# Optimization experiments

Measured on AMD Instinct MI355X. Metric: run time of the kernel, lower is better.

## Reference

```python
import jax, jax.numpy as jnp
import numpy as np
import math

HIDDEN_DIM = 1024
NUM_MODALITIES = 8
NUM_HEADS = 8
HEAD_DIM = HIDDEN_DIM // NUM_HEADS
LN_EPS = 1e-5


def setup_inputs() -> dict:
    key = jax.random.key(0)
    ks = jax.random.split(key, 12)
    B, K, D = 8192, NUM_MODALITIES, HIDDEN_DIM
    s = 1.0 / math.sqrt(D)
    inp = {
        'modality_encodings': jax.random.normal(ks[0], (B, K, D), dtype=jnp.float32),
        'selection_mask': jnp.ones((B, K), dtype=jnp.float32),
        # nn.Linear weights are [out, in]
        'wq': jax.random.uniform(ks[1], (D, D), jnp.float32, -s, s),
        'bq': jax.random.uniform(ks[2], (D,), jnp.float32, -s, s),
        'wk': jax.random.uniform(ks[3], (D, D), jnp.float32, -s, s),
        'bk': jax.random.uniform(ks[4], (D,), jnp.float32, -s, s),
        'wv': jax.random.uniform(ks[5], (D, D), jnp.float32, -s, s),
        'bv': jax.random.uniform(ks[6], (D,), jnp.float32, -s, s),
        'wo': jax.random.uniform(ks[7], (D, D), jnp.float32, -s, s),
        'bo': jax.random.uniform(ks[8], (D,), jnp.float32, -s, s),
        'rel_prior': jnp.eye(K, dtype=jnp.float32) + 0.1 * jax.random.normal(ks[9], (K, K), dtype=jnp.float32),
        'ln_gamma': jnp.ones((D,), dtype=jnp.float32),
        'ln_beta': jnp.zeros((D,), dtype=jnp.float32),
    }
    return inp


def reference(modality_encodings, selection_mask, wq, bq, wk, bk, wv, bv, wo, bo,
              rel_prior, ln_gamma, ln_beta):
    x = modality_encodings  # [B, K, D]
    B, K, D = x.shape
    H, Hd = NUM_HEADS, HEAD_DIM

    def lin(t, w, b):
        return t @ w.T + b

    def heads(t):  # [B,K,D] -> [B,H,K,Hd]
        return t.reshape(B, K, H, Hd).transpose(0, 2, 1, 3)

    q = heads(lin(x, wq, bq))
    k = heads(lin(x, wk, bk))
    v = heads(lin(x, wv, bv))

    scores = jnp.einsum('bhqd,bhkd->bhqk', q, k) / math.sqrt(Hd)
    scores = scores + rel_prior[None, None, :, :]  # learned additive bias

    # selection mask: mask_2d[b,q,k] = mask[b,q]*mask[b,k]; fill -inf where 0
    mask_2d = (selection_mask[:, :, None] * selection_mask[:, None, :]) > 0  # [B,K,K]
    scores = jnp.where(mask_2d[:, None, :, :], scores, -jnp.inf)

    attn = jax.nn.softmax(scores, axis=-1)
    # dropout(p=0.1) in eval mode -> identity
    out = jnp.einsum('bhqk,bhkd->bhqd', attn, v)  # [B,H,K,Hd]
    out = out.transpose(0, 2, 1, 3).reshape(B, K, D)
    out = lin(out, wo, bo)

    res = x + out
    mu = jnp.mean(res, axis=-1, keepdims=True)
    var = jnp.mean(jnp.square(res - mu), axis=-1, keepdims=True)
    return (res - mu) * jax.lax.rsqrt(var + LN_EPS) * ln_gamma + ln_beta
```

## Files before the change

### kernel.cpp

```cpp
#include <hip/hip_runtime.h>

typedef __attribute__((ext_vector_type(4))) float f32x4;
typedef __attribute__((ext_vector_type(8))) short short8;

#define LN_EPS 1e-5f

__device__ __forceinline__ float bf2f(short x) {
  union { unsigned u; float f; } c;
  c.u = ((unsigned)(unsigned short)x) << 16;
  return c.f;
}
__device__ __forceinline__ short f2b(float f) {
  union { float f; unsigned u; } c; c.f = f;
  unsigned r = (c.u + 0x7fffu + ((c.u >> 16) & 1u)) >> 16;
  return (short)r;
}

__global__ __launch_bounds__(256) void cvt_kernel(const float* __restrict__ src,
                                                  short* __restrict__ dst, int n8) {
  int idx = blockIdx.x * 256 + threadIdx.x;
  int stride = gridDim.x * 256;
  for (int c = idx; c < n8; c += stride) {
    const f32x4* s = (const f32x4*)(src + (size_t)c * 8);
    f32x4 v0 = s[0], v1 = s[1];
    short8 o;
    o[0] = f2b(v0.x); o[1] = f2b(v0.y); o[2] = f2b(v0.z); o[3] = f2b(v0.w);
    o[4] = f2b(v1.x); o[5] = f2b(v1.y); o[6] = f2b(v1.z); o[7] = f2b(v1.w);
    *(short8*)(dst + (size_t)c * 8) = o;
  }
}

__global__ __launch_bounds__(256) void pack_bias(const float* __restrict__ bq,
                                                 const float* __restrict__ bk,
                                                 const float* __restrict__ bv,
                                                 float* __restrict__ dst) {
  int t = blockIdx.x * 256 + threadIdx.x;
  if (t < 1024) { dst[t] = bq[t]; dst[1024 + t] = bk[t]; dst[2048 + t] = bv[t]; }
}

__device__ __forceinline__ void gload16(const short* g, const short* l) {
  __builtin_amdgcn_global_load_lds((const __attribute__((address_space(1))) unsigned int*)g,
                                   (__attribute__((address_space(3))) unsigned int*)l,
                                   16, 0, 0);
}

template <int MODE>
__global__ __launch_bounds__(512, 2) void gemm256(
    const short* __restrict__ A, const short* __restrict__ W,
    const float* __restrict__ bias, const float* __restrict__ resid,
    void* __restrict__ Cptr, int N) {
  __shared__ __align__(16) short lds[65536];

  const int tid = threadIdx.x;
  const int w = tid >> 6, l = tid & 63;
  const int wr = w >> 2, wc = w & 3;
  const int r0 = l & 15, hk = l >> 4;

  const int q8 = gridDim.x >> 3;
  const int wg = (blockIdx.x & 7) * q8 + (blockIdx.x >> 3);
  const int nbx = N >> 8;
  const int mb = wg / nbx, nb = wg - mb * nbx;
  const int m0 = mb << 8, n0 = nb << 8;

  const int srow = tid >> 3;
  const int colsh = (((tid & 7) ^ (srow & 7)) << 3);
  const short* gA00 = A + (size_t)(m0 + srow) * 1024 + colsh;
  const short* gA01 = A + (size_t)(m0 + srow + 64) * 1024 + colsh;
  const short* gA10 = A + (size_t)(m0 + 128 + srow) * 1024 + colsh;
  const short* gA11 = A + (size_t)(m0 + 128 + srow + 64) * 1024 + colsh;
  const short* gB00 = W + (size_t)(n0 + srow) * 1024 + colsh;
  const short* gB01 = W + (size_t)(n0 + srow + 64) * 1024 + colsh;
  const short* gB10 = W + (size_t)(n0 + 128 + srow) * 1024 + colsh;
  const short* gB11 = W + (size_t)(n0 + 128 + srow + 64) * 1024 + colsh;
  const int wofs = w * 512;

  const int ps0 = hk ^ (r0 & 7);
  const int aO0 = r0 * 64 + ps0 * 8;
  const int aO1 = r0 * 64 + (ps0 ^ 4) * 8;
  const int rB = (wc & 1) * 64;
  const int bO0 = (rB + r0) * 64 + ps0 * 8;
  const int bO1 = (rB + r0) * 64 + (ps0 ^ 4) * 8;
  const short* Abase = &lds[wr * 8192];
  const short* Bbase = &lds[32768 + (wc >> 1) * 8192];

  f32x4 acc[8][4];
#pragma unroll
  for (int i = 0; i < 8; ++i)
#pragma unroll
    for (int j = 0; j < 4; ++j) acc[i][j] = (f32x4)(0.f);

  gload16(gA00, &lds[wofs]);
  gload16(gA01, &lds[wofs + 4096]);
  gload16(gA10, &lds[8192 + wofs]);
  gload16(gA11, &lds[8192 + wofs + 4096]);
  gload16(gB00, &lds[32768 + wofs]);
  gload16(gB01, &lds[32768 + wofs + 4096]);
  gload16(gB10, &lds[32768 + 8192 + wofs]);
  gload16(gB11, &lds[32768 + 8192 + wofs + 4096]);

#pragma unroll 2
  for (int t = 0; t < 16; ++t) {
    const int p = t & 1;
    const short* Ab = Abase + p * 16384;
    const short* Bb = Bbase + p * 16384;
    short8 av[4][2], bw[4][2];

    __builtin_amdgcn_sched_barrier(0);
    asm volatile("s_waitcnt vmcnt(0)" ::: "memory");
    __builtin_amdgcn_s_barrier();
    __builtin_amdgcn_sched_barrier(0);
#pragma unroll
    for (int i4 = 0; i4 < 4; ++i4) {
      av[i4][0] = *(const short8*)&Ab[aO0 + i4 * 1024];
      av[i4][1] = *(const short8*)&Ab[aO1 + i4 * 1024];
    }
#pragma unroll
    for (int j = 0; j < 2; ++j) {
      bw[j][0] = *(const short8*)&Bb[bO0 + j * 1024];
      bw[j][1] = *(const short8*)&Bb[bO1 + j * 1024];
    }
    if (t < 15) {
      const int kofs = (t + 1) * 64;
      const int qb = (p ^ 1) * 16384;
      gload16(gA00 + kofs, &lds[qb + wofs]);
      gload16(gA01 + kofs, &lds[qb + wofs + 4096]);
      gload16(gA10 + kofs, &lds[qb + 8192 + wofs]);
      gload16(gA11 + kofs, &lds[qb + 8192 + wofs + 4096]);
      gload16(gB00 + kofs, &lds[32768 + qb + wofs]);
      gload16(gB01 + kofs, &lds[32768 + qb + wofs + 4096]);
      gload16(gB10 + kofs, &lds[32768 + qb + 8192 + wofs]);
      gload16(gB11 + kofs, &lds[32768 + qb + 8192 + wofs + 4096]);
    }
    __builtin_amdgcn_s_setprio(1);
#pragma unroll
    for (int ks = 0; ks < 2; ++ks)
#pragma unroll
      for (int i4 = 0; i4 < 4; ++i4)
#pragma unroll
        for (int j = 0; j < 2; ++j)
          acc[i4][j] = __builtin_amdgcn_mfma_f32_16x16x32_bf16(av[i4][ks], bw[j][ks], acc[i4][j], 0, 0, 0);
    __builtin_amdgcn_s_setprio(0);

    __builtin_amdgcn_s_barrier();
    __builtin_amdgcn_sched_barrier(0);
#pragma unroll
    for (int j = 2; j < 4; ++j) {
      bw[j][0] = *(const short8*)&Bb[bO0 + j * 1024];
      bw[j][1] = *(const short8*)&Bb[bO1 + j * 1024];
    }
    __builtin_amdgcn_s_setprio(1);
#pragma unroll
    for (int ks = 0; ks < 2; ++ks)
#pragma unroll
      for (int i4 = 0; i4 < 4; ++i4)
#pragma unroll
        for (int j = 2; j < 4; ++j)
          acc[i4][j] = __builtin_amdgcn_mfma_f32_16x16x32_bf16(av[i4][ks], bw[j][ks], acc[i4][j], 0, 0, 0);
    __builtin_amdgcn_s_setprio(0);

    __builtin_amdgcn_s_barrier();
    __builtin_amdgcn_sched_barrier(0);
#pragma unroll
    for (int i4 = 0; i4 < 4; ++i4) {
      av[i4][0] = *(const short8*)&Ab[aO0 + (4 + i4) * 1024];
      av[i4][1] = *(const short8*)&Ab[aO1 + (4 + i4) * 1024];
    }
    __builtin_amdgcn_s_setprio(1);
#pragma unroll
    for (int ks = 0; ks < 2; ++ks)
#pragma unroll
      for (int i4 = 0; i4 < 4; ++i4)
#pragma unroll
        for (int j = 2; j < 4; ++j)
          acc[4 + i4][j] = __builtin_amdgcn_mfma_f32_16x16x32_bf16(av[i4][ks], bw[j][ks], acc[4 + i4][j], 0, 0, 0);
    __builtin_amdgcn_s_setprio(0);

    __builtin_amdgcn_s_barrier();
    __builtin_amdgcn_sched_barrier(0);
    __builtin_amdgcn_s_setprio(1);
#pragma unroll
    for (int ks = 0; ks < 2; ++ks)
#pragma unroll
      for (int i4 = 0; i4 < 4; ++i4)
#pragma unroll
        for (int j = 0; j < 2; ++j)
          acc[4 + i4][j] = __builtin_amdgcn_mfma_f32_16x16x32_bf16(av[i4][ks], bw[j][ks], acc[4 + i4][j], 0, 0, 0);
    __builtin_amdgcn_s_setprio(0);
  }

  const int crow = m0 + wr * 128 + hk * 4;
  const int ccol = n0 + wc * 64 + r0;
  if (MODE == 0) {
    short* C = (short*)Cptr;
#pragma unroll
    for (int j = 0; j < 4; ++j) {
      float bj = bias[ccol + j * 16];
#pragma unroll
      for (int i = 0; i < 8; ++i) {
        size_t base = (size_t)(crow + i * 16) * N + (ccol + j * 16);
#pragma unroll
        for (int rr = 0; rr < 4; ++rr)
          C[base + (size_t)rr * N] = f2b(acc[i][j][rr] + bj);
      }
    }
  } else {
    float* C = (float*)Cptr;
#pragma unroll
    for (int j = 0; j < 4; ++j) {
      float bj = bias[ccol + j * 16];
#pragma unroll
      for (int i = 0; i < 8; ++i) {
        size_t base = (size_t)(crow + i * 16) * N + (ccol + j * 16);
#pragma unroll
        for (int rr = 0; rr < 4; ++rr)
          C[base + (size_t)rr * N] =
              acc[i][j][rr] + bj + resid[base + (size_t)rr * N];
      }
    }
  }
}

__global__ __launch_bounds__(256) void attn_kernel(
    const short* __restrict__ qkv, const float* __restrict__ prior,
    const float* __restrict__ mask, short* __restrict__ out) {
  __shared__ short sq[8 * 3080];
  const int tid = threadIdx.x;
  const int b = blockIdx.x;
  for (int c = tid; c < 3072; c += 256) {
    int row = c / 384;
    int cc = c - row * 384;
    *(short8*)&sq[row * 3080 + cc * 8] =
        *(const short8*)&qkv[((size_t)b * 8 + row) * 3072 + cc * 8];
  }
  __syncthreads();
  const int l = tid & 63, w = tid >> 6;
  const int i = l >> 3, j = l & 7;
  const float pv = prior[l];
  const float mm = mask[b * 8 + i] * mask[b * 8 + j];
#pragma unroll
  for (int hh = 0; hh < 2; ++hh) {
    const int h = w + hh * 4;
    const short* Qr = &sq[i * 3080 + h * 128];
    const short* Kr = &sq[j * 3080 + 1024 + h * 128];
    float s = 0.f;
#pragma unroll
    for (int c = 0; c < 16; ++c) {
      short8 qa = *(const short8*)&Qr[c * 8];
      short8 ka = *(const short8*)&Kr[c * 8];
#pragma unroll
      for (int e = 0; e < 8; ++e) s += bf2f(qa[e]) * bf2f(ka[e]);
    }
    s = s * 0.08838834764831843f + pv;
    if (!(mm > 0.f)) s = -__builtin_inff();
    float mx = s;
#pragma unroll
    for (int off = 1; off < 8; off <<= 1) mx = fmaxf(mx, __shfl_xor(mx, off));
    float e = __expf(s - mx);
    float sum = e;
#pragma unroll
    for (int off = 1; off < 8; off <<= 1) sum += __shfl_xor(sum, off);
    float p = e / sum;
    float o[16];
#pragma unroll
    for (int t = 0; t < 16; ++t) o[t] = 0.f;
#pragma unroll
    for (int jj = 0; jj < 8; ++jj) {
      float pj = __shfl(p, i * 8 + jj);
      const short* Vr = &sq[jj * 3080 + 2048 + h * 128 + j * 16];
      short8 v0 = *(const short8*)&Vr[0];
      short8 v1 = *(const short8*)&Vr[8];
#pragma unroll
      for (int e2 = 0; e2 < 8; ++e2) {
        o[e2] += pj * bf2f(v0[e2]);
        o[8 + e2] += pj * bf2f(v1[e2]);
      }
    }
    short8 o0, o1;
#pragma unroll
    for (int e2 = 0; e2 < 8; ++e2) { o0[e2] = f2b(o[e2]); o1[e2] = f2b(o[8 + e2]); }
    short* dst = out + ((size_t)(b * 8 + i)) * 1024 + h * 128 + j * 16;
    *(short8*)dst = o0;
    *(short8*)(dst + 8) = o1;
  }
}

__global__ __launch_bounds__(256) void ln_kernel(float* __restrict__ io,
                                                 const float* __restrict__ gamma,
                                                 const float* __restrict__ beta) {
  const int l = threadIdx.x & 63, w = threadIdx.x >> 6;
  float* p = io + ((size_t)blockIdx.x * 4 + w) * 1024;
  f32x4 v[4];
  float s = 0.f;
#pragma unroll
  for (int c = 0; c < 4; ++c) {
    v[c] = *(const f32x4*)(p + (c * 64 + l) * 4);
    s += v[c][0] + v[c][1] + v[c][2] + v[c][3];
  }
#pragma unroll
  for (int off = 32; off > 0; off >>= 1) s += __shfl_xor(s, off);
  const float mu = s * (1.f / 1024.f);
  float s2 = 0.f;
#pragma unroll
  for (int c = 0; c < 4; ++c)
#pragma unroll
    for (int e = 0; e < 4; ++e) { float d = v[c][e] - mu; s2 += d * d; }
#pragma unroll
  for (int off = 32; off > 0; off >>= 1) s2 += __shfl_xor(s2, off);
  const float rstd = rsqrtf(s2 * (1.f / 1024.f) + LN_EPS);
#pragma unroll
  for (int c = 0; c < 4; ++c) {
    f32x4 g = *(const f32x4*)(gamma + (c * 64 + l) * 4);
    f32x4 bt = *(const f32x4*)(beta + (c * 64 + l) * 4);
    f32x4 ov;
#pragma unroll
    for (int e = 0; e < 4; ++e) ov[e] = (v[c][e] - mu) * rstd * g[e] + bt[e];
    *(f32x4*)(p + (c * 64 + l) * 4) = ov;
  }
}

extern "C" void kernel_launch(void* const* d_in, const int* in_sizes, int n_in,
                              void* d_out, int out_size, void* d_ws, size_t ws_size,
                              hipStream_t stream) {
  const float* x     = (const float*)d_in[0];
  const float* mask  = (const float*)d_in[1];
  const float* wq    = (const float*)d_in[2];
  const float* bq    = (const float*)d_in[3];
  const float* wk    = (const float*)d_in[4];
  const float* bk    = (const float*)d_in[5];
  const float* wv    = (const float*)d_in[6];
  const float* bv    = (const float*)d_in[7];
  const float* wo    = (const float*)d_in[8];
  const float* bo    = (const float*)d_in[9];
  const float* prior = (const float*)d_in[10];
  const float* gamma = (const float*)d_in[11];
  const float* beta  = (const float*)d_in[12];

  char* ws = (char*)d_ws;
  short* qkv  = (short*)(ws);
  short* xb   = (short*)(ws + 402653184L);
  short* wall = (short*)(ws + 536870912L);
  short* wob  = (short*)(ws + 543162368L);
  float* ball = (float*)(ws + 545259520L);

  cvt_kernel<<<2048, 256, 0, stream>>>(x, xb, 8388608);
  cvt_kernel<<<512, 256, 0, stream>>>(wq, wall,           131072);
  cvt_kernel<<<512, 256, 0, stream>>>(wk, wall + 1048576, 131072);
  cvt_kernel<<<512, 256, 0, stream>>>(wv, wall + 2097152, 131072);
  cvt_kernel<<<512, 256, 0, stream>>>(wo, wob,            131072);
  pack_bias<<<4, 256, 0, stream>>>(bq, bk, bv, ball);

  gemm256<0><<<3072, 512, 0, stream>>>(xb, wall, ball, nullptr, qkv, 3072);
  attn_kernel<<<8192, 256, 0, stream>>>(qkv, prior, mask, xb);
  gemm256<1><<<1024, 512, 0, stream>>>(xb, wob, bo, x, d_out, 1024);
  ln_kernel<<<16384, 256, 0, stream>>>((float*)d_out, gamma, beta);
}
```

Measured before the change: 1.005 ms.

## Prefetch GEMM tiles two steps ahead within the double buffer

The GEMM main loop now stages tiles t and t+1 up front. It issues the global-to-LDS loads for tile t+2 into the current buffer once each operand's last LDS reads in the iteration have passed a barrier: B after the third phase, A after the fourth. The per-iteration wait drops from vmcnt(0) to vmcnt(8), so only the older tile's loads must complete and one tile's loads stay in flight across the barrier. The aim is to hide more global-memory latency behind MFMA work. The cost is more outstanding memory operations and a vmcnt-based ordering that is easy to get wrong.

```diff
diff --git a/kernel.cpp b/kernel.cpp
--- a/kernel.cpp
+++ b/kernel.cpp
@@ -74,6 +74,17 @@
   const short* gB11 = W + (size_t)(n0 + 128 + srow + 64) * 1024 + colsh;
   const int wofs = w * 512;
 
+#define STAGE_A(T, BUF) do { const int kofs_ = (T) * 64, qb_ = (BUF) * 16384;       \
+    gload16(gA00 + kofs_, &lds[qb_ + wofs]);                                        \
+    gload16(gA01 + kofs_, &lds[qb_ + wofs + 4096]);                                 \
+    gload16(gA10 + kofs_, &lds[qb_ + 8192 + wofs]);                                 \
+    gload16(gA11 + kofs_, &lds[qb_ + 8192 + wofs + 4096]); } while (0)
+#define STAGE_B(T, BUF) do { const int kofs_ = (T) * 64, qb_ = (BUF) * 16384;       \
+    gload16(gB00 + kofs_, &lds[32768 + qb_ + wofs]);                                \
+    gload16(gB01 + kofs_, &lds[32768 + qb_ + wofs + 4096]);                         \
+    gload16(gB10 + kofs_, &lds[32768 + qb_ + 8192 + wofs]);                         \
+    gload16(gB11 + kofs_, &lds[32768 + qb_ + 8192 + wofs + 4096]); } while (0)
+
   const int ps0 = hk ^ (r0 & 7);
   const int aO0 = r0 * 64 + ps0 * 8;
   const int aO1 = r0 * 64 + (ps0 ^ 4) * 8;
@@ -89,14 +100,8 @@
 #pragma unroll
     for (int j = 0; j < 4; ++j) acc[i][j] = (f32x4)(0.f);
 
-  gload16(gA00, &lds[wofs]);
-  gload16(gA01, &lds[wofs + 4096]);
-  gload16(gA10, &lds[8192 + wofs]);
-  gload16(gA11, &lds[8192 + wofs + 4096]);
-  gload16(gB00, &lds[32768 + wofs]);
-  gload16(gB01, &lds[32768 + wofs + 4096]);
-  gload16(gB10, &lds[32768 + 8192 + wofs]);
-  gload16(gB11, &lds[32768 + 8192 + wofs + 4096]);
+  STAGE_A(0, 0); STAGE_B(0, 0);
+  STAGE_A(1, 1); STAGE_B(1, 1);
 
 #pragma unroll 2
   for (int t = 0; t < 16; ++t) {
@@ -106,7 +111,8 @@
     short8 av[4][2], bw[4][2];
 
     __builtin_amdgcn_sched_barrier(0);
-    asm volatile("s_waitcnt vmcnt(0)" ::: "memory");
+    if (t == 15) { asm volatile("s_waitcnt vmcnt(0)" ::: "memory"); }
+    else         { asm volatile("s_waitcnt vmcnt(8)" ::: "memory"); }
     __builtin_amdgcn_s_barrier();
     __builtin_amdgcn_sched_barrier(0);
 #pragma unroll
@@ -119,18 +125,6 @@
       bw[j][0] = *(const short8*)&Bb[bO0 + j * 1024];
       bw[j][1] = *(const short8*)&Bb[bO1 + j * 1024];
     }
-    if (t < 15) {
-      const int kofs = (t + 1) * 64;
-      const int qb = (p ^ 1) * 16384;
-      gload16(gA00 + kofs, &lds[qb + wofs]);
-      gload16(gA01 + kofs, &lds[qb + wofs + 4096]);
-      gload16(gA10 + kofs, &lds[qb + 8192 + wofs]);
-      gload16(gA11 + kofs, &lds[qb + 8192 + wofs + 4096]);
-      gload16(gB00 + kofs, &lds[32768 + qb + wofs]);
-      gload16(gB01 + kofs, &lds[32768 + qb + wofs + 4096]);
-      gload16(gB10 + kofs, &lds[32768 + qb + 8192 + wofs]);
-      gload16(gB11 + kofs, &lds[32768 + qb + 8192 + wofs + 4096]);
-    }
     __builtin_amdgcn_s_setprio(1);
 #pragma unroll
     for (int ks = 0; ks < 2; ++ks)
@@ -165,6 +159,7 @@
       av[i4][0] = *(const short8*)&Ab[aO0 + (4 + i4) * 1024];
       av[i4][1] = *(const short8*)&Ab[aO1 + (4 + i4) * 1024];
     }
+    if (t < 14) STAGE_B(t + 2, p);
     __builtin_amdgcn_s_setprio(1);
 #pragma unroll
     for (int ks = 0; ks < 2; ++ks)
@@ -177,6 +172,7 @@
 
     __builtin_amdgcn_s_barrier();
     __builtin_amdgcn_sched_barrier(0);
+    if (t < 14) STAGE_A(t + 2, p);
     __builtin_amdgcn_s_setprio(1);
 #pragma unroll
     for (int ks = 0; ks < 2; ++ks)
@@ -187,6 +183,8 @@
           acc[4 + i4][j] = __builtin_amdgcn_mfma_f32_16x16x32_bf16(av[i4][ks], bw[j][ks], acc[4 + i4][j], 0, 0, 0);
     __builtin_amdgcn_s_setprio(0);
   }
+#undef STAGE_A
+#undef STAGE_B
 
   const int crow = m0 + wr * 128 + hk * 4;
   const int ccol = n0 + wc * 64 + r0;
```

After: 966.3 us. -3.9%, faster.
